# Optimization experiments

Hardware: AMD Instinct MI355X
Metric: run time of the kernel (lower is better)

## Reference

```python
import jax, jax.numpy as jnp
import numpy as np

NUM_HEADS = 16
DIM = 1024
B, L = 2, 2048
NEG = -10000000000.0


def setup_inputs() -> dict:
    key = jax.random.key(0)
    ks = jax.random.split(key, 8)
    queries = jax.random.normal(ks[0], (B, L, DIM), dtype=jnp.float32)
    keys = jax.random.normal(ks[1], (B, L, DIM), dtype=jnp.float32)
    values = jax.random.normal(ks[2], (B, L, DIM), dtype=jnp.float32)
    mask = jax.random.uniform(ks[3], (B, L, L)) < 0.1
    s = 1.0 / np.sqrt(DIM)
    Wq = jax.random.uniform(ks[4], (DIM, DIM), minval=-s, maxval=s, dtype=jnp.float32)
    Wk = jax.random.uniform(ks[5], (DIM, DIM), minval=-s, maxval=s, dtype=jnp.float32)
    Wv = jax.random.uniform(ks[6], (DIM, DIM), minval=-s, maxval=s, dtype=jnp.float32)
    Wo = jax.random.uniform(ks[7], (DIM, DIM), minval=-s, maxval=s, dtype=jnp.float32)
    return {"queries": queries, "keys": keys, "values": values, "mask": mask,
            "Wq": Wq, "Wk": Wk, "Wv": Wv, "Wo": Wo}


def reference(queries, keys, values, mask, Wq, Wk, Wv, Wo):
    b, l, d = queries.shape
    h = NUM_HEADS
    dk = d // h
    # torch Linear(bias=False): y = x @ W.T ; then view(b, l, dk, h) -> head axis LAST
    qs = (queries @ Wq.T).reshape(b, l, dk, h)
    ks = (keys @ Wk.T).reshape(b, l, dk, h)
    vs = (values @ Wv.T).reshape(b, l, dk, h)
    # routing is None in the live code path
    w = jnp.einsum('bidh,bodh->bioh', qs, ks) / jnp.sqrt(jnp.asarray(dk, jnp.float32))
    w = jnp.where(mask[..., None], NEG, w)          # masked_fill where mask True
    w = jax.nn.softmax(w, axis=-2)                   # softmax over key axis 'o'
    mha = jnp.einsum('bioh,bodh->bidh', w, vs).reshape(b, l, d)
    # dropout is identity in eval mode
    return mha @ Wo.T
```

## Files before the change

kernel.cpp:

```cpp
#include <hip/hip_runtime.h>
#include <hip/hip_bf16.h>
#include <cstdint>
#include <cstddef>

typedef unsigned short ushort_t;
typedef __attribute__((ext_vector_type(8))) short short8;
typedef __attribute__((ext_vector_type(8))) unsigned short ushort8;
typedef __attribute__((ext_vector_type(4))) unsigned short ushort4v;
typedef __attribute__((ext_vector_type(4))) float f32x4;
typedef __attribute__((ext_vector_type(2))) unsigned long long ull2;
typedef __attribute__((ext_vector_type(2))) unsigned int uint2v;

#define LPAD 72

__device__ __forceinline__ unsigned short f2bf(float f) {
    unsigned int x = __float_as_uint(f);
    unsigned int r = x + 0x7fffu + ((x >> 16) & 1u);
    return (unsigned short)(r >> 16);
}

__device__ __forceinline__ unsigned int cvt_pk_bf16(float lo, float hi) {
    unsigned int r;
    asm("v_cvt_pk_bf16_f32 %0, %1, %2" : "=v"(r) : "v"(lo), "v"(hi));
    return r;
}

__device__ __forceinline__ void async16(const ushort_t* g, ushort_t* l) {
    __builtin_amdgcn_global_load_lds(
        (const __attribute__((address_space(1))) unsigned int*)g,
        (__attribute__((address_space(3))) unsigned int*)l,
        16, 0, 0);
}

__global__ __launch_bounds__(256) void cvt(const float* __restrict__ q,
                                           const float* __restrict__ k,
                                           const float* __restrict__ v,
                                           const float* __restrict__ Wq,
                                           const float* __restrict__ Wk,
                                           const float* __restrict__ Wv,
                                           ushort_t* __restrict__ qb,
                                           ushort_t* __restrict__ kb,
                                           ushort_t* __restrict__ vb,
                                           ushort_t* __restrict__ Wqb,
                                           ushort_t* __restrict__ Wkb,
                                           ushort_t* __restrict__ Wvb) {
    const int z = blockIdx.y;
    const float* X = (z == 0) ? q : (z == 1) ? k : v;
    const float* W = (z == 0) ? Wq : (z == 1) ? Wk : Wv;
    ushort_t* Xo = (z == 0) ? qb : (z == 1) ? kb : vb;
    ushort_t* Wo2 = (z == 0) ? Wqb : (z == 1) ? Wkb : Wvb;
    const size_t idx = (((size_t)blockIdx.x << 8) + threadIdx.x) << 3;
    const float* src; ushort_t* dst; float sc = 1.0f;
    if (idx < 4194304) { src = X + idx; dst = Xo + idx; if (z == 0) sc = 0.125f; }
    else               { src = W + (idx - 4194304); dst = Wo2 + (idx - 4194304); }
    f32x4 a0 = *(const f32x4*)src, a1 = *(const f32x4*)(src + 4);
    ushort8 o;
    #pragma unroll
    for (int j = 0; j < 4; j++) { o[j] = f2bf(a0[j] * sc); o[j + 4] = f2bf(a1[j] * sc); }
    *(ushort8*)dst = o;
}

__global__ __launch_bounds__(256) void maskbits_kernel(const int* __restrict__ mask,
                                                       unsigned long long* __restrict__ Mbits) {
    const int row  = blockIdx.x;
    const int w    = threadIdx.x >> 6;
    const int lane = threadIdx.x & 63;
    const int* mrow = mask + (size_t)row * 2048;
    #pragma unroll
    for (int it = 0; it < 8; it++) {
        const int o = (it << 8) + (w << 6) + lane;
        const unsigned long long bb = __ballot(mrow[o] != 0);
        if (lane == 0) Mbits[(size_t)((it << 2) + w) * 4096 + row] = bb;
    }
}

__global__ __launch_bounds__(256) void woswz(const float* __restrict__ W,
                                             ushort_t* __restrict__ WoH) {
    __shared__ float row[1024 + 64];
    const int j = blockIdx.x, t = threadIdx.x;
    f32x4 v = *(const f32x4*)(W + (size_t)j * 1024 + (t << 2));
    #pragma unroll
    for (int s = 0; s < 4; s++) { const int c = (t << 2) + s; row[c + (c >> 4)] = v[s]; }
    __syncthreads();
    #pragma unroll
    for (int s = 0; s < 4; s++) {
        const int k = t + (s << 8);
        const int col = ((k & 63) << 4) + (k >> 6);
        WoH[(size_t)j * 1024 + k] = f2bf(row[col + (col >> 4)]);
    }
}

__global__ __launch_bounds__(256) void gemm_proj(const ushort_t* __restrict__ qb,
                                                 const ushort_t* __restrict__ kb,
                                                 const ushort_t* __restrict__ vb,
                                                 const ushort_t* __restrict__ Wqb,
                                                 const ushort_t* __restrict__ Wkb,
                                                 const ushort_t* __restrict__ Wvb,
                                                 ushort_t* __restrict__ Qh,
                                                 ushort_t* __restrict__ Kh,
                                                 ushort_t* __restrict__ VhT) {
    __shared__ ushort_t Xs[2][4096];
    __shared__ ushort_t Ws[2][4096];

    const int lid  = blockIdx.x;
    const int nIdx = lid / 96;
    const int rem  = lid % 96;
    const int z    = rem >> 5;
    const int mIdx = rem & 31;
    const int n0   = nIdx << 7;
    const int m0   = mIdx << 7;

    const ushort_t* Xb = (z == 0) ? qb : (z == 1) ? kb : vb;
    const ushort_t* Wb = (z == 0) ? Wqb : (z == 1) ? Wkb : Wvb;

    const int tid  = threadIdx.x;
    const int w    = tid >> 6;
    const int lane = tid & 63;
    const int lm   = lane & 15;
    const int quad = lane >> 4;
    const int wm   = w & 1;
    const int wn   = w >> 1;

    f32x4 acc[4][4];
    #pragma unroll
    for (int i = 0; i < 4; i++)
        #pragma unroll
        for (int j = 0; j < 4; j++) acc[i][j] = (f32x4){0.f, 0.f, 0.f, 0.f};

    auto stage = [&](int k0, int buf) {
        #pragma unroll
        for (int i = 0; i < 2; i++) {
            const int L   = (((w << 1) + i) << 6) + lane;
            const int c4  = L >> 7, row = L & 127;
            const int lb  = (((w << 1) + i) << 6) << 3;
            async16(Xb + (size_t)(m0 + row) * 1024 + k0 + (c4 << 3), &Xs[buf][lb]);
            async16(Wb + (size_t)(n0 + row) * 1024 + k0 + (c4 << 3), &Ws[buf][lb]);
        }
    };

    stage(0, 0);
    __syncthreads();

    int cur = 0;
    for (int t = 0; t < 32; ++t) {
        if (t < 31) stage((t + 1) << 5, cur ^ 1);
        short8 af[4], bf4[4];
        #pragma unroll
        for (int mf = 0; mf < 4; mf++)
            af[mf] = *(const short8*)&Xs[cur][((quad << 7) + (wm << 6) + (mf << 4) + lm) << 3];
        #pragma unroll
        for (int nf = 0; nf < 4; nf++)
            bf4[nf] = *(const short8*)&Ws[cur][((quad << 7) + (wn << 6) + (nf << 4) + lm) << 3];
        #pragma unroll
        for (int mf = 0; mf < 4; mf++)
            #pragma unroll
            for (int nf = 0; nf < 4; nf++)
                acc[mf][nf] = __builtin_amdgcn_mfma_f32_16x16x32_bf16(af[mf], bf4[nf], acc[mf][nf], 0, 0, 0);
        if (t < 31) { __syncthreads(); cur ^= 1; }
    }

    const int bb    = m0 >> 11;
    const int l0    = m0 & 2047;
    const int dbase = (n0 >> 4) + (wn << 2);
    if (z != 2) {
        ushort_t* OUT = (z == 0) ? Qh : Kh;
        #pragma unroll
        for (int mf = 0; mf < 4; mf++)
            #pragma unroll
            for (int r = 0; r < 4; r++) {
                const int row = (wm << 6) + (mf << 4) + (quad << 2) + r;
                ushort4v o = { f2bf(acc[mf][0][r]), f2bf(acc[mf][1][r]),
                               f2bf(acc[mf][2][r]), f2bf(acc[mf][3][r]) };
                *(ushort4v*)(OUT + ((size_t)((bb << 4) + lm) * 2048 + l0 + row) * 64 + dbase) = o;
            }
    } else {
        #pragma unroll
        for (int mf = 0; mf < 4; mf++)
            #pragma unroll
            for (int nf = 0; nf < 4; nf++) {
                const int lbase = l0 + (wm << 6) + (mf << 4) + (quad << 2);
                ushort4v o = { f2bf(acc[mf][nf][0]), f2bf(acc[mf][nf][1]),
                               f2bf(acc[mf][nf][2]), f2bf(acc[mf][nf][3]) };
                *(ushort4v*)(VhT + ((size_t)((bb << 4) + lm) * 64 + dbase + nf) * 2048 + lbase) = o;
            }
    }
}

__global__ __launch_bounds__(256) void gemm_out(const ushort_t* __restrict__ mhaH,
                                                const ushort_t* __restrict__ WoH,
                                                float* __restrict__ C) {
    __shared__ ushort_t Xs[2][4096];
    __shared__ ushort_t Ws[2][2048];

    const int lid  = blockIdx.x;
    const int mIdx = ((lid & 7) << 2) | ((lid >> 3) & 3);
    const int nIdx = lid >> 5;
    const int m0   = mIdx << 7;
    const int n0   = nIdx << 6;

    const int tid  = threadIdx.x;
    const int w    = tid >> 6;
    const int lane = tid & 63;
    const int lm   = lane & 15;
    const int quad = lane >> 4;
    const int wm   = w & 1;
    const int wn   = w >> 1;
    const int ab   = m0 >> 11;
    const int al0  = m0 & 2047;

    f32x4 acc[4][2];
    #pragma unroll
    for (int i = 0; i < 4; i++)
        #pragma unroll
        for (int j = 0; j < 2; j++) acc[i][j] = (f32x4){0.f, 0.f, 0.f, 0.f};

    auto stage = [&](int k0, int buf) {
        const int h  = k0 >> 6;
        const int d0 = k0 & 63;
        #pragma unroll
        for (int i = 0; i < 2; i++) {
            const int L   = (i << 8) + (w << 6) + lane;
            const int c4  = L >> 7, row = L & 127;
            async16(mhaH + ((size_t)(ab * 16 + h) * 2048 + al0 + row) * 64 + d0 + (c4 << 3),
                    &Xs[buf][((i << 8) + (w << 6)) << 3]);
        }
        {
            const int L   = (w << 6) + lane;
            const int c4  = L >> 6, row = L & 63;
            async16(WoH + (size_t)(n0 + row) * 1024 + k0 + (c4 << 3),
                    &Ws[buf][(w << 6) << 3]);
        }
    };

    stage(0, 0);
    __syncthreads();

    int cur = 0;
    for (int t = 0; t < 32; ++t) {
        if (t < 31) stage((t + 1) << 5, cur ^ 1);
        short8 af[4], bf2[2];
        #pragma unroll
        for (int mf = 0; mf < 4; mf++)
            af[mf] = *(const short8*)&Xs[cur][((quad << 7) + (wm << 6) + (mf << 4) + lm) << 3];
        #pragma unroll
        for (int nf = 0; nf < 2; nf++)
            bf2[nf] = *(const short8*)&Ws[cur][((quad << 6) + (wn << 5) + (nf << 4) + lm) << 3];
        #pragma unroll
        for (int mf = 0; mf < 4; mf++)
            #pragma unroll
            for (int nf = 0; nf < 2; nf++)
                acc[mf][nf] = __builtin_amdgcn_mfma_f32_16x16x32_bf16(af[mf], bf2[nf], acc[mf][nf], 0, 0, 0);
        if (t < 31) { __syncthreads(); cur ^= 1; }
    }
    #pragma unroll
    for (int mf = 0; mf < 4; mf++)
        #pragma unroll
        for (int nf = 0; nf < 2; nf++)
            #pragma unroll
            for (int r = 0; r < 4; r++) {
                const int row = m0 + (wm << 6) + (mf << 4) + (quad << 2) + r;
                const int col = n0 + (wn << 5) + (nf << 4) + lm;
                C[(size_t)row * 1024 + col] = acc[mf][nf][r];
            }
}

__global__ __launch_bounds__(256, 2) void flash_attn(const ushort_t* __restrict__ Qh,
                                                     const ushort_t* __restrict__ Kh,
                                                     const ushort_t* __restrict__ VhT,
                                                     const unsigned long long* __restrict__ Mbits,
                                                     ushort_t* __restrict__ mhaH) {
    __shared__ ushort_t Ks[2][4096];
    __shared__ ushort_t Vs[2][4096];
    __shared__ ushort_t Pw[4][16 * LPAD];

    const int tid  = threadIdx.x;
    const int w    = tid >> 6;
    const int lane = tid & 63;
    const int lm   = lane & 15;
    const int quad = lane >> 4;
    const int lid  = blockIdx.x;
    const int bh   = ((lid & 7) << 2) | ((lid >> 3) & 3);
    const int q0   = (lid >> 5) << 7;
    const int b    = bh >> 4;

    const ushort_t* Qb  = Qh  + ((size_t)bh << 17);
    const ushort_t* Kb  = Kh  + ((size_t)bh << 17);
    const ushort_t* Vtb = VhT + ((size_t)bh << 17);

    short8 aq[2][2];
    #pragma unroll
    for (int g = 0; g < 2; g++) {
        const ushort_t* qp = Qb + (size_t)(q0 + (w << 5) + (g << 4) + lm) * 64 + (quad << 3);
        aq[g][0] = *(const short8*)qp;
        aq[g][1] = *(const short8*)(qp + 32);
    }

    float l_part[2][4] = {{0.f,0.f,0.f,0.f},{0.f,0.f,0.f,0.f}};
    f32x4 o_acc[2][4] = {{{0.f,0.f,0.f,0.f},{0.f,0.f,0.f,0.f},{0.f,0.f,0.f,0.f},{0.f,0.f,0.f,0.f}},
                         {{0.f,0.f,0.f,0.f},{0.f,0.f,0.f,0.f},{0.f,0.f,0.f,0.f},{0.f,0.f,0.f,0.f}}};

    const int rowbase  = (b << 11) + q0 + (w << 5);
    const int shamt    = (lm & 7) << 2;
    const bool hi_half = lm >= 8;

    const ushort_t* ksrc = Kb  + (size_t)((lm << 2) + w) * 64 + (quad << 3);
    const ushort_t* vsrc = Vtb + (size_t)((w << 4) + lm) * 2048 + (quad << 3);

    auto stageKV = [&](int kt0, int buf) {
        async16(ksrc + (size_t)kt0 * 64,      &Ks[buf][((w << 7)     ) << 3]);
        async16(ksrc + (size_t)kt0 * 64 + 32, &Ks[buf][((w << 7) + 64) << 3]);
        async16(vsrc + kt0,      &Vs[buf][((w << 7)     ) << 3]);
        async16(vsrc + kt0 + 32, &Vs[buf][((w << 7) + 64) << 3]);
    };

    stageKV(0, 0);
    __syncthreads();

    int cur = 0;
    for (int t = 0; t < 32; ++t) {
        const int kt0 = t << 6;
        if (t < 31) stageKV(kt0 + 64, cur ^ 1);

        short8 bk[4][2], bv[4][2];
        #pragma unroll
        for (int c = 0; c < 4; c++) {
            bk[c][0] = *(const short8*)&Ks[cur][((c << 7) + lane) << 3];
            bk[c][1] = *(const short8*)&Ks[cur][((c << 7) + 64 + lane) << 3];
            bv[c][0] = *(const short8*)&Vs[cur][((c << 7) + lane) << 3];
            bv[c][1] = *(const short8*)&Vs[cur][((c << 7) + 64 + lane) << 3];
        }

        const unsigned long long* Mt = Mbits + (size_t)(kt0 >> 6) * 4096 + rowbase;

        #pragma unroll
        for (int g = 0; g < 2; g++) {
            f32x4 s[4];
            #pragma unroll
            for (int c = 0; c < 4; c++) {
                f32x4 zz = {0.f, 0.f, 0.f, 0.f};
                zz = __builtin_amdgcn_mfma_f32_16x16x32_bf16(aq[g][0], bk[c][0], zz, 0, 0, 0);
                zz = __builtin_amdgcn_mfma_f32_16x16x32_bf16(aq[g][1], bk[c][1], zz, 0, 0, 0);
                s[c] = zz;
            }
            unsigned long long mb[4];
            {
                const unsigned long long* mp = Mt + (g << 4) + (quad << 2);
                ull2 t0 = *(const ull2*)mp;
                ull2 t1 = *(const ull2*)(mp + 2);
                mb[0] = t0[0]; mb[1] = t0[1]; mb[2] = t1[0]; mb[3] = t1[1];
            }
            #pragma unroll
            for (int r = 0; r < 4; r++) {
                const unsigned long long m64 = mb[r];
                const unsigned word = hi_half ? (unsigned)(m64 >> 32) : (unsigned)m64;
                const unsigned nib  = (word >> shamt) & 0xFu;
                float p0 = __expf(s[0][r]); if (nib & 1u) p0 = 0.f;
                float p1 = __expf(s[1][r]); if (nib & 2u) p1 = 0.f;
                float p2 = __expf(s[2][r]); if (nib & 4u) p2 = 0.f;
                float p3 = __expf(s[3][r]); if (nib & 8u) p3 = 0.f;
                l_part[g][r] += (p0 + p1) + (p2 + p3);
                uint2v pv2;
                pv2[0] = cvt_pk_bf16(p0, p1);
                pv2[1] = cvt_pk_bf16(p2, p3);
                *(uint2v*)&Pw[w][((quad << 2) + r) * LPAD + (lm << 2)] = pv2;
            }
            short8 ap0 = *(const short8*)&Pw[w][lm * LPAD + (quad << 3)];
            short8 ap1 = *(const short8*)&Pw[w][lm * LPAD + 32 + (quad << 3)];
            #pragma unroll
            for (int cd = 0; cd < 4; cd++) {
                o_acc[g][cd] = __builtin_amdgcn_mfma_f32_16x16x32_bf16(ap0, bv[cd][0], o_acc[g][cd], 0, 0, 0);
                o_acc[g][cd] = __builtin_amdgcn_mfma_f32_16x16x32_bf16(ap1, bv[cd][1], o_acc[g][cd], 0, 0, 0);
            }
        }
        if (t < 31) { __syncthreads(); cur ^= 1; }
    }

    #pragma unroll
    for (int g = 0; g < 2; g++) {
        #pragma unroll
        for (int r = 0; r < 4; r++) {
            float l = l_part[g][r];
            l += __shfl_xor(l, 1, 64);
            l += __shfl_xor(l, 2, 64);
            l += __shfl_xor(l, 4, 64);
            l += __shfl_xor(l, 8, 64);
            const float inv_l = 1.0f / l;
            const int i = q0 + (w << 5) + (g << 4) + (quad << 2) + r;
            ushort_t* orow = mhaH + (((size_t)bh * 2048 + i) << 6);
            #pragma unroll
            for (int cd = 0; cd < 4; cd++)
                orow[(cd << 4) + lm] = f2bf(o_acc[g][cd][r] * inv_l);
        }
    }
}

extern "C" void kernel_launch(void* const* d_in, const int* in_sizes, int n_in,
                              void* d_out, int out_size, void* d_ws, size_t ws_size,
                              hipStream_t stream) {
    const float* q    = (const float*)d_in[0];
    const float* k    = (const float*)d_in[1];
    const float* v    = (const float*)d_in[2];
    const int*   mask = (const int*)d_in[3];
    const float* Wq   = (const float*)d_in[4];
    const float* Wk   = (const float*)d_in[5];
    const float* Wv   = (const float*)d_in[6];
    const float* Wo   = (const float*)d_in[7];
    float* out = (float*)d_out;

    ushort_t* qb   = (ushort_t*)d_ws;
    ushort_t* kb   = qb  + 4194304;
    ushort_t* vb   = kb  + 4194304;
    ushort_t* Wqb  = vb  + 4194304;
    ushort_t* Wkb  = Wqb + 1048576;
    ushort_t* Wvb  = Wkb + 1048576;
    ushort_t* Qh   = Wvb + 1048576;
    ushort_t* Kh   = Qh  + 4194304;
    ushort_t* VhT  = Kh  + 4194304;
    ushort_t* mhaH = qb;
    ushort_t* WoH  = kb;
    unsigned long long* Mbits = (unsigned long long*)(kb + 1048576);

    dim3 gb(256);
    cvt<<<dim3(2560, 3), gb, 0, stream>>>(q, k, v, Wq, Wk, Wv, qb, kb, vb, Wqb, Wkb, Wvb);
    gemm_proj<<<dim3(768), gb, 0, stream>>>(qb, kb, vb, Wqb, Wkb, Wvb, Qh, Kh, VhT);
    maskbits_kernel<<<dim3(4096), gb, 0, stream>>>(mask, Mbits);
    woswz<<<dim3(1024), gb, 0, stream>>>(Wo, WoH);
    flash_attn<<<dim3(512), gb, 0, stream>>>(Qh, Kh, VhT, Mbits, mhaH);
    gemm_out<<<dim3(512), gb, 0, stream>>>(mhaH, WoH, out);
}
```

Measured before the change: 324.1 us.

## Triple-buffer async LDS loads with partial vmcnt waits across all three kernels

Moves the projection GEMM, output GEMM and attention kernels from double to triple LDS buffering. Each stage is issued two iterations ahead, and the full __syncthreads is replaced by s_waitcnt vmcnt(N) plus a barrier, so the next tile's global loads can stay in flight. The attention kernel also hoists the mask-bit loads ahead of staging, batches the QK MFMAs for both row groups before the softmax, double-indexes the P scratch per group, and raises wave priority around the MFMA blocks. This costs more LDS, which may lower occupancy, and the hand-counted vmcnt values must match the number of loads in flight, including the mask loads.

```diff
diff --git a/kernel.cpp b/kernel.cpp
--- a/kernel.cpp
+++ b/kernel.cpp
@@ -12,6 +12,12 @@
 typedef __attribute__((ext_vector_type(2))) unsigned int uint2v;
 
 #define LPAD 72
+
+#define PIPE_WAIT_BAR(N) do {                                              \
+    asm volatile("s_waitcnt vmcnt(" #N ") lgkmcnt(0)" ::: "memory");       \
+    __builtin_amdgcn_s_barrier();                                          \
+    asm volatile("" ::: "memory");                                         \
+} while (0)
 
 __device__ __forceinline__ unsigned short f2bf(float f) {
     unsigned int x = __float_as_uint(f);
@@ -99,8 +105,8 @@
                                                  ushort_t* __restrict__ Qh,
                                                  ushort_t* __restrict__ Kh,
                                                  ushort_t* __restrict__ VhT) {
-    __shared__ ushort_t Xs[2][4096];
-    __shared__ ushort_t Ws[2][4096];
+    __shared__ ushort_t Xs[3][4096];
+    __shared__ ushort_t Ws[3][4096];
 
     const int lid  = blockIdx.x;
     const int nIdx = lid / 96;
@@ -139,11 +145,13 @@
     };
 
     stage(0, 0);
-    __syncthreads();
+    stage(32, 1);
+    PIPE_WAIT_BAR(4);
 
     int cur = 0;
     for (int t = 0; t < 32; ++t) {
-        if (t < 31) stage((t + 1) << 5, cur ^ 1);
+        int nb = cur + 2; if (nb >= 3) nb -= 3;
+        if (t < 30) stage((t + 2) << 5, nb);
         short8 af[4], bf4[4];
         #pragma unroll
         for (int mf = 0; mf < 4; mf++)
@@ -156,7 +164,9 @@
             #pragma unroll
             for (int nf = 0; nf < 4; nf++)
                 acc[mf][nf] = __builtin_amdgcn_mfma_f32_16x16x32_bf16(af[mf], bf4[nf], acc[mf][nf], 0, 0, 0);
-        if (t < 31) { __syncthreads(); cur ^= 1; }
+        if (t < 30)       PIPE_WAIT_BAR(4);
+        else if (t == 30) PIPE_WAIT_BAR(0);
+        cur += 1; if (cur == 3) cur = 0;
     }
 
     const int bb    = m0 >> 11;
@@ -189,8 +199,8 @@
 __global__ __launch_bounds__(256) void gemm_out(const ushort_t* __restrict__ mhaH,
                                                 const ushort_t* __restrict__ WoH,
                                                 float* __restrict__ C) {
-    __shared__ ushort_t Xs[2][4096];
-    __shared__ ushort_t Ws[2][2048];
+    __shared__ ushort_t Xs[3][4096];
+    __shared__ ushort_t Ws[3][2048];
 
     const int lid  = blockIdx.x;
     const int mIdx = ((lid & 7) << 2) | ((lid >> 3) & 3);
@@ -233,11 +243,13 @@
     };
 
     stage(0, 0);
-    __syncthreads();
+    stage(32, 1);
+    PIPE_WAIT_BAR(3);
 
     int cur = 0;
     for (int t = 0; t < 32; ++t) {
-        if (t < 31) stage((t + 1) << 5, cur ^ 1);
+        int nb = cur + 2; if (nb >= 3) nb -= 3;
+        if (t < 30) stage((t + 2) << 5, nb);
         short8 af[4], bf2[2];
         #pragma unroll
         for (int mf = 0; mf < 4; mf++)
@@ -250,7 +262,9 @@
             #pragma unroll
             for (int nf = 0; nf < 2; nf++)
                 acc[mf][nf] = __builtin_amdgcn_mfma_f32_16x16x32_bf16(af[mf], bf2[nf], acc[mf][nf], 0, 0, 0);
-        if (t < 31) { __syncthreads(); cur ^= 1; }
+        if (t < 30)       PIPE_WAIT_BAR(3);
+        else if (t == 30) PIPE_WAIT_BAR(0);
+        cur += 1; if (cur == 3) cur = 0;
     }
     #pragma unroll
     for (int mf = 0; mf < 4; mf++)
@@ -269,9 +283,9 @@
                                                      const ushort_t* __restrict__ VhT,
                                                      const unsigned long long* __restrict__ Mbits,
                                                      ushort_t* __restrict__ mhaH) {
-    __shared__ ushort_t Ks[2][4096];
-    __shared__ ushort_t Vs[2][4096];
-    __shared__ ushort_t Pw[4][16 * LPAD];
+    __shared__ ushort_t Ks[3][4096];
+    __shared__ ushort_t Vs[3][4096];
+    __shared__ ushort_t Pw[4][2][16 * LPAD];
 
     const int tid  = threadIdx.x;
     const int w    = tid >> 6;
@@ -314,12 +328,25 @@
     };
 
     stageKV(0, 0);
-    __syncthreads();
+    stageKV(64, 1);
+    PIPE_WAIT_BAR(4);
 
     int cur = 0;
     for (int t = 0; t < 32; ++t) {
         const int kt0 = t << 6;
-        if (t < 31) stageKV(kt0 + 64, cur ^ 1);
+        int nb = cur + 2; if (nb >= 3) nb -= 3;
+
+        const unsigned long long* Mt = Mbits + (size_t)(kt0 >> 6) * 4096 + rowbase;
+        unsigned long long mb[2][4];
+        #pragma unroll
+        for (int g = 0; g < 2; g++) {
+            const unsigned long long* mp = Mt + (g << 4) + (quad << 2);
+            ull2 t0 = *(const ull2*)mp;
+            ull2 t1 = *(const ull2*)(mp + 2);
+            mb[g][0] = t0[0]; mb[g][1] = t0[1]; mb[g][2] = t1[0]; mb[g][3] = t1[1];
+        }
+
+        if (t < 30) stageKV(kt0 + 128, nb);
 
         short8 bk[4][2], bv[4][2];
         #pragma unroll
@@ -330,49 +357,54 @@
             bv[c][1] = *(const short8*)&Vs[cur][((c << 7) + 64 + lane) << 3];
         }
 
-        const unsigned long long* Mt = Mbits + (size_t)(kt0 >> 6) * 4096 + rowbase;
-
-        #pragma unroll
-        for (int g = 0; g < 2; g++) {
-            f32x4 s[4];
+        f32x4 s[2][4];
+        __builtin_amdgcn_s_setprio(1);
+        #pragma unroll
+        for (int g = 0; g < 2; g++)
             #pragma unroll
             for (int c = 0; c < 4; c++) {
                 f32x4 zz = {0.f, 0.f, 0.f, 0.f};
                 zz = __builtin_amdgcn_mfma_f32_16x16x32_bf16(aq[g][0], bk[c][0], zz, 0, 0, 0);
                 zz = __builtin_amdgcn_mfma_f32_16x16x32_bf16(aq[g][1], bk[c][1], zz, 0, 0, 0);
-                s[c] = zz;
-            }
-            unsigned long long mb[4];
-            {
-                const unsigned long long* mp = Mt + (g << 4) + (quad << 2);
-                ull2 t0 = *(const ull2*)mp;
-                ull2 t1 = *(const ull2*)(mp + 2);
-                mb[0] = t0[0]; mb[1] = t0[1]; mb[2] = t1[0]; mb[3] = t1[1];
-            }
+                s[g][c] = zz;
+            }
+        __builtin_amdgcn_s_setprio(0);
+
+        #pragma unroll
+        for (int g = 0; g < 2; g++) {
             #pragma unroll
             for (int r = 0; r < 4; r++) {
-                const unsigned long long m64 = mb[r];
+                const unsigned long long m64 = mb[g][r];
                 const unsigned word = hi_half ? (unsigned)(m64 >> 32) : (unsigned)m64;
                 const unsigned nib  = (word >> shamt) & 0xFu;
-                float p0 = __expf(s[0][r]); if (nib & 1u) p0 = 0.f;
-                float p1 = __expf(s[1][r]); if (nib & 2u) p1 = 0.f;
-                float p2 = __expf(s[2][r]); if (nib & 4u) p2 = 0.f;
-                float p3 = __expf(s[3][r]); if (nib & 8u) p3 = 0.f;
+                float p0 = __expf(s[g][0][r]); if (nib & 1u) p0 = 0.f;
+                float p1 = __expf(s[g][1][r]); if (nib & 2u) p1 = 0.f;
+                float p2 = __expf(s[g][2][r]); if (nib & 4u) p2 = 0.f;
+                float p3 = __expf(s[g][3][r]); if (nib & 8u) p3 = 0.f;
                 l_part[g][r] += (p0 + p1) + (p2 + p3);
                 uint2v pv2;
                 pv2[0] = cvt_pk_bf16(p0, p1);
                 pv2[1] = cvt_pk_bf16(p2, p3);
-                *(uint2v*)&Pw[w][((quad << 2) + r) * LPAD + (lm << 2)] = pv2;
-            }
-            short8 ap0 = *(const short8*)&Pw[w][lm * LPAD + (quad << 3)];
-            short8 ap1 = *(const short8*)&Pw[w][lm * LPAD + 32 + (quad << 3)];
+                *(uint2v*)&Pw[w][g][((quad << 2) + r) * LPAD + (lm << 2)] = pv2;
+            }
+        }
+
+        __builtin_amdgcn_s_setprio(1);
+        #pragma unroll
+        for (int g = 0; g < 2; g++) {
+            short8 ap0 = *(const short8*)&Pw[w][g][lm * LPAD + (quad << 3)];
+            short8 ap1 = *(const short8*)&Pw[w][g][lm * LPAD + 32 + (quad << 3)];
             #pragma unroll
             for (int cd = 0; cd < 4; cd++) {
                 o_acc[g][cd] = __builtin_amdgcn_mfma_f32_16x16x32_bf16(ap0, bv[cd][0], o_acc[g][cd], 0, 0, 0);
                 o_acc[g][cd] = __builtin_amdgcn_mfma_f32_16x16x32_bf16(ap1, bv[cd][1], o_acc[g][cd], 0, 0, 0);
             }
         }
-        if (t < 31) { __syncthreads(); cur ^= 1; }
+        __builtin_amdgcn_s_setprio(0);
+
+        if (t < 30)       PIPE_WAIT_BAR(4);
+        else if (t == 30) PIPE_WAIT_BAR(0);
+        cur += 1; if (cur == 3) cur = 0;
     }
 
     #pragma unroll
```

After: 311.7 us. 3.8% less time.
